# Optimization experiments

Measured on AMD Instinct MI355X. Metric: run time of the kernel, lower is better.

Reference implementation:

```python
import jax, jax.numpy as jnp
import numpy as np

B, L, D, H = 8, 256, 512, 512
NEG_BIG = 1e8  # matches the 100000000.0 mask constant in the original


def setup_inputs() -> dict:
    key = jax.random.key(0)
    k1, k2, k3, k4 = jax.random.split(key, 4)
    enc = jax.random.normal(k1, (B, L, D), dtype=jnp.float32)
    # Glorot-uniform init, matching tf.keras.initializers.GlorotUniform
    s_w = float(np.sqrt(6.0 / (D + H)))
    W_l = jax.random.uniform(k2, (D, H), jnp.float32, -s_w, s_w)
    W_r = jax.random.uniform(k3, (D, H), jnp.float32, -s_w, s_w)
    s_u = float(np.sqrt(6.0 / (H + H)))  # 1-D glorot: fan_in = fan_out = H
    U = jax.random.uniform(k4, (H,), jnp.float32, -s_u, s_u)
    logit_bias = jnp.zeros((1,), jnp.float32)  # bias_initial_value=None -> zeros init
    return {"encoder_output": enc, "W_l": W_l, "W_r": W_r, "U": U, "logit_bias": logit_bias}


def reference(encoder_output, W_l, W_r, U, logit_bias):
    # dot_l[b,i,h], dot_r[b,j,h]
    dot_l = jnp.einsum('bik,kh->bih', encoder_output, W_l)
    dot_r = jnp.einsum('bjk,kh->bjh', encoder_output, W_r)
    # additive biaffine: tanh(dot_l_i + dot_r_j) . U  -> logits[b,i,j]
    final_sum = jnp.tanh(dot_l[:, :, None, :] + dot_r[:, None, :, :])  # [B,L,L,H]
    logits = jnp.einsum('bijh,h->bij', final_sum, U) + logit_bias[0]   # [B,L,L]
    # per-row self-mask (one_hot(i)) applied over all rows at once
    masked = logits - NEG_BIG * jnp.eye(L, dtype=logits.dtype)[None]   # [B,L,L]
    # original returns python lists over i of [B,L]; stack -> [L,B,L]
    mask_scores = jnp.transpose(masked, (1, 0, 2))
    p = jax.nn.sigmoid(mask_scores)
    samples = jax.random.bernoulli(jax.random.key(42), p).astype(jnp.int32)  # [L,B,L]
    # Bernoulli entropy from logits x: p*softplus(-x) + (1-p)*softplus(x)
    entropy = p * jax.nn.softplus(-mask_scores) + (1.0 - p) * jax.nn.softplus(mask_scores)
    return samples, mask_scores, entropy
```

## Files before the change

kernel.cpp:

```cpp
#include <hip/hip_runtime.h>
#include <stdint.h>

#define Bb 8
#define Ll 256
#define Dd 512
#define Hh 512
#define Nout (Ll * Bb * Ll)

#define Kc 2.8853900817779268

#define RNG_PARTITIONABLE 1

typedef __attribute__((ext_vector_type(8))) short bf16x8;
typedef __attribute__((ext_vector_type(4))) float f32x4;


__device__ __forceinline__ uint32_t rotl32(uint32_t v, int s) {
  return (v << s) | (v >> (32 - s));
}
__device__ __forceinline__ void tf_round(uint32_t& x0, uint32_t& x1, int r) {
  x0 += x1;
  x1 = rotl32(x1, r);
  x1 ^= x0;
}
__device__ __forceinline__ uint2 threefry2x32_k042(uint32_t x0, uint32_t x1) {
  const uint32_t k0 = 0u;
  const uint32_t k1 = 42u;
  const uint32_t k2 = 0x1BD11BDAu ^ k0 ^ k1;
  x0 += k0; x1 += k1;
  tf_round(x0, x1, 13); tf_round(x0, x1, 15); tf_round(x0, x1, 26); tf_round(x0, x1, 6);
  x0 += k1; x1 += k2 + 1u;
  tf_round(x0, x1, 17); tf_round(x0, x1, 29); tf_round(x0, x1, 16); tf_round(x0, x1, 24);
  x0 += k2; x1 += k0 + 2u;
  tf_round(x0, x1, 13); tf_round(x0, x1, 15); tf_round(x0, x1, 26); tf_round(x0, x1, 6);
  x0 += k0; x1 += k1 + 3u;
  tf_round(x0, x1, 17); tf_round(x0, x1, 29); tf_round(x0, x1, 16); tf_round(x0, x1, 24);
  x0 += k1; x1 += k2 + 4u;
  tf_round(x0, x1, 13); tf_round(x0, x1, 15); tf_round(x0, x1, 26); tf_round(x0, x1, 6);
  x0 += k2; x1 += k0 + 5u;
  return make_uint2(x0, x1);
}

__device__ __forceinline__ uint32_t rng_bits(uint32_t n) {
#if RNG_PARTITIONABLE
  uint2 o = threefry2x32_k042(0u, n);
  return o.x ^ o.y;
#else
  const uint32_t half = (uint32_t)(Nout / 2);
  if (n < half) {
    uint2 o = threefry2x32_k042(n, n + half);
    return o.x;
  } else {
    uint2 o = threefry2x32_k042(n - half, n);
    return o.y;
  }
#endif
}

__device__ __forceinline__ unsigned short bf16_rne(float f) {
  uint32_t u = __float_as_uint(f);
  u = (u + 0x7fffu + ((u >> 16) & 1u)) >> 16;
  return (unsigned short)u;
}
__device__ __forceinline__ float bf16_tof(unsigned short h) {
  return __uint_as_float(((uint32_t)h) << 16);
}
__device__ __forceinline__ void split3(float a, unsigned short& h,
                                       unsigned short& m, unsigned short& l) {
  h = bf16_rne(a);
  const float r1 = a - bf16_tof(h);
  m = bf16_rne(r1);
  const float r2 = r1 - bf16_tof(m);
  l = bf16_rne(r2);
}

__device__ __forceinline__ uint32_t fp_off(int r, int k) {
  const int mt = r >> 4, l15 = r & 15;
  const int kc = k >> 5, kq = (k >> 3) & 3, j = k & 7;
  return (uint32_t)(mt * 8192 + kc * 512 + kq * 128 + l15 * 8 + j);
}

__global__ __launch_bounds__(256) void split_enc(
    const float* __restrict__ enc, unsigned short* __restrict__ ah,
    unsigned short* __restrict__ am, unsigned short* __restrict__ al) {
  const int idx = (blockIdx.x * 256 + threadIdx.x) * 4;
  const int r = idx >> 9;
  const int k = idx & 511;
  const float4 v = *(const float4*)(enc + idx);
  ushort4 h4, m4, l4;
  split3(v.x, h4.x, m4.x, l4.x);
  split3(v.y, h4.y, m4.y, l4.y);
  split3(v.z, h4.z, m4.z, l4.z);
  split3(v.w, h4.w, m4.w, l4.w);
  const uint32_t o = fp_off(r, k);
  *(ushort4*)(ah + o) = h4;
  *(ushort4*)(am + o) = m4;
  *(ushort4*)(al + o) = l4;
}

__global__ __launch_bounds__(256) void split_wt(
    const float* __restrict__ Wl, const float* __restrict__ Wr,
    unsigned short* __restrict__ wh, unsigned short* __restrict__ wm,
    unsigned short* __restrict__ wl) {
  const int z = blockIdx.z;
  const float* W = z ? Wr : Wl;
  const uint32_t zo = (uint32_t)z * Hh * Dd;
  const int k0 = blockIdx.x * 64;
  const int n0 = blockIdx.y * 64;
  __shared__ float tile[64][65];

  const int t = threadIdx.x;
#pragma unroll
  for (int rep = 0; rep < 4; ++rep) {
    const int idx = t + rep * 256;
    const int r = idx >> 4;
    const int c = (idx & 15) * 4;
    const float4 v = *(const float4*)(W + (size_t)(k0 + r) * Hh + n0 + c);
    tile[r][c + 0] = v.x; tile[r][c + 1] = v.y;
    tile[r][c + 2] = v.z; tile[r][c + 3] = v.w;
  }
  __syncthreads();
#pragma unroll
  for (int rep = 0; rep < 4; ++rep) {
    const int idx = t + rep * 256;
    const int rr = idx >> 4;
    const int cc = (idx & 15) * 4;
    ushort4 h4, m4, l4;
    split3(tile[cc + 0][rr], h4.x, m4.x, l4.x);
    split3(tile[cc + 1][rr], h4.y, m4.y, l4.y);
    split3(tile[cc + 2][rr], h4.z, m4.z, l4.z);
    split3(tile[cc + 3][rr], h4.w, m4.w, l4.w);
    const uint32_t o = zo + fp_off(n0 + rr, k0 + cc);
    *(ushort4*)(wh + o) = h4;
    *(ushort4*)(wm + o) = m4;
    *(ushort4*)(wl + o) = l4;
  }
}

__global__ __launch_bounds__(256) void gemm_mfma(
    const unsigned short* __restrict__ ah, const unsigned short* __restrict__ am,
    const unsigned short* __restrict__ al, const unsigned short* __restrict__ wh,
    const unsigned short* __restrict__ wm, const unsigned short* __restrict__ wl,
    float* __restrict__ el, float* __restrict__ er) {
  const int flat = blockIdx.x;
  const int xcd = flat & 7;
  const int loc = flat >> 3;
  const int z = loc >> 5;
  const int ni = (loc >> 2) & 7;
  const int mi = (xcd << 2) | (loc & 3);
  float* C = z ? er : el;
  const int m0 = mi * 64;
  const int n0 = ni * 64;

  __shared__ unsigned short Asm[2][12 * 512];
  __shared__ unsigned short Bsm[2][12 * 512];

  const int t = threadIdx.x;
  const int lane = t & 63;
  const int wv = t >> 6;
  const int l15 = lane & 15;

  const unsigned short* gp[6];
  uint32_t go[6];
  int lq[6];
  bool isA[6];
#pragma unroll
  for (int s = 0; s < 6; ++s) {
    const int q = wv * 6 + s;
    if (q < 12) {
      const int p = q >> 2, mt = q & 3;
      gp[s] = (p == 0) ? ah : (p == 1) ? am : al;
      go[s] = (uint32_t)(mi * 4 + mt) * 8192u + (uint32_t)lane * 8u;
      lq[s] = q * 512;
      isA[s] = true;
    } else {
      const int q2 = q - 12;
      const int p = q2 >> 2, nt = q2 & 3;
      gp[s] = (p == 0) ? wh : (p == 1) ? wm : wl;
      go[s] = (uint32_t)z * 262144u + (uint32_t)(ni * 4 + nt) * 8192u +
              (uint32_t)lane * 8u;
      lq[s] = q2 * 512;
      isA[s] = false;
    }
  }

  auto stage = [&](int buf, int kc) {
    const uint32_t k0 = (uint32_t)kc * 512u;
#pragma unroll
    for (int s = 0; s < 6; ++s) {
      unsigned short* dst = isA[s] ? &Asm[buf][lq[s]] : &Bsm[buf][lq[s]];
      __builtin_amdgcn_global_load_lds(
          (const __attribute__((address_space(1))) void*)(gp[s] + go[s] + k0),
          (__attribute__((address_space(3))) void*)dst, 16, 0, 0);
    }
  };

  const int mp = wv & 1;
  const int np = wv >> 1;

  f32x4 acc[2][2][2];
#pragma unroll
  for (int mi2 = 0; mi2 < 2; ++mi2)
#pragma unroll
    for (int ni2 = 0; ni2 < 2; ++ni2)
#pragma unroll
      for (int hf = 0; hf < 2; ++hf) acc[mi2][ni2][hf] = (f32x4){0.f, 0.f, 0.f, 0.f};

  stage(0, 0);
  __syncthreads();

  for (int kc = 0; kc < 16; ++kc) {
    const int buf = kc & 1;
    if (kc < 15) stage(buf ^ 1, kc + 1);

    bf16x8 af[2][3], bfr[2][3];
#pragma unroll
    for (int mi2 = 0; mi2 < 2; ++mi2)
#pragma unroll
      for (int p = 0; p < 3; ++p)
        af[mi2][p] = *(const bf16x8*)&Asm[buf][(p * 4 + mp * 2 + mi2) * 512 + lane * 8];
#pragma unroll
    for (int ni2 = 0; ni2 < 2; ++ni2)
#pragma unroll
      for (int p = 0; p < 3; ++p)
        bfr[ni2][p] = *(const bf16x8*)&Bsm[buf][(p * 4 + np * 2 + ni2) * 512 + lane * 8];

    const int hf = kc >> 3;
#pragma unroll
    for (int mi2 = 0; mi2 < 2; ++mi2)
#pragma unroll
      for (int ni2 = 0; ni2 < 2; ++ni2) {
        f32x4 A = acc[mi2][ni2][hf];
        A = __builtin_amdgcn_mfma_f32_16x16x32_bf16(af[mi2][0], bfr[ni2][0], A, 0, 0, 0);
        A = __builtin_amdgcn_mfma_f32_16x16x32_bf16(af[mi2][0], bfr[ni2][1], A, 0, 0, 0);
        A = __builtin_amdgcn_mfma_f32_16x16x32_bf16(af[mi2][1], bfr[ni2][0], A, 0, 0, 0);
        A = __builtin_amdgcn_mfma_f32_16x16x32_bf16(af[mi2][0], bfr[ni2][2], A, 0, 0, 0);
        A = __builtin_amdgcn_mfma_f32_16x16x32_bf16(af[mi2][2], bfr[ni2][0], A, 0, 0, 0);
        A = __builtin_amdgcn_mfma_f32_16x16x32_bf16(af[mi2][1], bfr[ni2][1], A, 0, 0, 0);
        acc[mi2][ni2][hf] = A;
      }
    __syncthreads();
  }

  const int rbase = (lane >> 4) * 4;
#pragma unroll
  for (int mi2 = 0; mi2 < 2; ++mi2) {
    const int mbase = m0 + (mp * 2 + mi2) * 16 + rbase;
#pragma unroll
    for (int ni2 = 0; ni2 < 2; ++ni2) {
      const int n = n0 + (np * 2 + ni2) * 16 + l15;
#pragma unroll
      for (int reg = 0; reg < 4; ++reg) {
        const double s = (double)acc[mi2][ni2][0][reg] + (double)acc[mi2][ni2][1][reg];
        C[(size_t)(mbase + reg) * Hh + n] = __builtin_amdgcn_exp2f((float)(Kc * s));
      }
    }
  }
}

__device__ __forceinline__ void group4_acc(float& S, const float4 a,
                                           const float4 bv, const float4 u) {
  const float d0 = __builtin_fmaf(a.x, bv.x, 1.0f);
  const float d1 = __builtin_fmaf(a.y, bv.y, 1.0f);
  const float d2 = __builtin_fmaf(a.z, bv.z, 1.0f);
  const float d3 = __builtin_fmaf(a.w, bv.w, 1.0f);
  const float p01 = d0 * d1;
  const float p23 = d2 * d3;
  const float D = p01 * p23;
  float n01 = u.x * d1;
  n01 = __builtin_fmaf(u.y, d0, n01);
  float n23 = u.z * d3;
  n23 = __builtin_fmaf(u.w, d2, n23);
  float num = n01 * p23;
  num = __builtin_fmaf(n23, p01, num);
  S = __builtin_fmaf(num, __builtin_amdgcn_rcpf(D), S);
}

__global__ __launch_bounds__(256) void biaffine_part(
    const float* __restrict__ el, const float* __restrict__ er,
    const float* __restrict__ U, float* __restrict__ part) {
  const int flat = blockIdx.x;
  const int b = flat & 7;
  const int loc = flat >> 3;
  const int ks = loc >> 4;
  const int ib = (loc >> 2) & 3;
  const int jb = loc & 3;
  const int i0 = ib * 64;
  const int j0 = jb * 64;
  const int h0 = ks * 64;

  __shared__ float els[64][68];
  __shared__ float ers[64][68];
  __shared__ float us[64];

  const int t = threadIdx.x;
  if (t < 16) *(float4*)&us[t * 4] = *(const float4*)(U + h0 + t * 4);

  const float* elg = el + (size_t)(b * Ll + i0) * Hh + h0;
  const float* erg = er + (size_t)(b * Ll + j0) * Hh + h0;
#pragma unroll
  for (int rep = 0; rep < 4; ++rep) {
    const int idx = t + rep * 256;
    const int r = idx >> 4;
    const int c = (idx & 15) * 4;
    *(float4*)&els[r][c] = *(const float4*)(elg + (size_t)r * Hh + c);
    *(float4*)&ers[r][c] = *(const float4*)(erg + (size_t)r * Hh + c);
  }
  __syncthreads();

  float usl = 0.0f;
#pragma unroll
  for (int q = 0; q < 16; ++q) {
    const float4 u = *(const float4*)&us[q * 4];
    usl += ((u.x + u.y) + u.z) + u.w;
  }

  const int ti = t >> 4;
  const int tj = t & 15;

  float S[4][4];
#pragma unroll
  for (int r = 0; r < 4; ++r)
#pragma unroll
    for (int c = 0; c < 4; ++c) S[r][c] = 0.0f;

  for (int g = 0; g < 16; ++g) {
    const int h = g * 4;
    const float4 u = *(const float4*)&us[h];
    float4 av[4], bv[4];
#pragma unroll
    for (int c = 0; c < 4; ++c) {
      av[c] = *(const float4*)&els[ti + 16 * c][h];
      bv[c] = *(const float4*)&ers[tj + 16 * c][h];
    }
#pragma unroll
    for (int r = 0; r < 4; ++r)
#pragma unroll
      for (int c = 0; c < 4; ++c) group4_acc(S[r][c], av[r], bv[c], u);
  }

  float* pslice = part + (size_t)ks * Nout;
#pragma unroll
  for (int r = 0; r < 4; ++r) {
    const int i = i0 + ti + 16 * r;
#pragma unroll
    for (int c = 0; c < 4; ++c) {
      const int j = j0 + tj + 16 * c;
      const uint32_t n = ((uint32_t)i * Bb + (uint32_t)b) * Ll + (uint32_t)j;
      pslice[n] = __builtin_fmaf(-2.0f, S[r][c], usl);
    }
  }
}

__global__ __launch_bounds__(256) void biaffine_emit(
    const float* __restrict__ part, const float* __restrict__ biasp,
    float* __restrict__ out) {
  const uint32_t n4 = (blockIdx.x * 256u + threadIdx.x) * 4u;
  double s0 = 0.0, s1 = 0.0, s2 = 0.0, s3 = 0.0;
#pragma unroll
  for (int k = 0; k < 8; ++k) {
    const float4 v = *(const float4*)(part + (size_t)k * Nout + n4);
    s0 += (double)v.x;
    s1 += (double)v.y;
    s2 += (double)v.z;
    s3 += (double)v.w;
  }
  const float bias = biasp[0];
  const double sv[4] = {s0, s1, s2, s3};

  float4 samp4, x4, ent4;
  float* sp = &samp4.x;
  float* xp = &x4.x;
  float* ep = &ent4.x;
#pragma unroll
  for (int q = 0; q < 4; ++q) {
    const uint32_t n = n4 + q;
    const int i = (int)(n >> 11);
    const int j = (int)(n & 255u);
    float x = (float)sv[q] + bias;
    if (i == j) x -= 1e8f;

    const double pd = 1.0 / (1.0 + exp(-(double)x));
    const float pf = (float)pd;

    const uint32_t bits = rng_bits(n);
    const float uu = __uint_as_float((bits >> 9) | 0x3f800000u) - 1.0f;
    sp[q] = (uu < pf) ? 1.0f : 0.0f;
    xp[q] = x;

    const float ax = fabsf(x);
    const float l1p = log1pf(expf(-ax));
    const float sp_pos = fmaxf(x, 0.0f) + l1p;
    const float sp_neg = fmaxf(-x, 0.0f) + l1p;
    ep[q] = pf * sp_neg + (1.0f - pf) * sp_pos;
  }
  *(float4*)(out + n4) = samp4;
  *(float4*)(out + Nout + n4) = x4;
  *(float4*)(out + 2 * (size_t)Nout + n4) = ent4;
}

extern "C" void kernel_launch(void* const* d_in, const int* in_sizes, int n_in,
                              void* d_out, int out_size, void* d_ws,
                              size_t ws_size, hipStream_t stream) {
  const float* enc = (const float*)d_in[0];
  const float* Wl = (const float*)d_in[1];
  const float* Wr = (const float*)d_in[2];
  const float* U = (const float*)d_in[3];
  const float* lb = (const float*)d_in[4];
  float* out = (float*)d_out;

  char* w = (char*)d_ws;
  float* el = (float*)w;                      w += (size_t)Bb * Ll * Hh * 4;
  float* er = (float*)w;                      w += (size_t)Bb * Ll * Hh * 4;
  float* part = (float*)w;                    w += (size_t)8 * Nout * 4;
  unsigned short* ah = (unsigned short*)w;    w += (size_t)Bb * Ll * Dd * 2;
  unsigned short* am = (unsigned short*)w;    w += (size_t)Bb * Ll * Dd * 2;
  unsigned short* al = (unsigned short*)w;    w += (size_t)Bb * Ll * Dd * 2;
  unsigned short* wh = (unsigned short*)w;    w += (size_t)2 * Dd * Hh * 2;
  unsigned short* wm = (unsigned short*)w;    w += (size_t)2 * Dd * Hh * 2;
  unsigned short* wl = (unsigned short*)w;    w += (size_t)2 * Dd * Hh * 2;

  split_enc<<<dim3((Bb * Ll * Dd) / 1024), 256, 0, stream>>>(enc, ah, am, al);
  split_wt<<<dim3(Dd / 64, Hh / 64, 2), 256, 0, stream>>>(Wl, Wr, wh, wm, wl);
  gemm_mfma<<<dim3(512, 1, 1), 256, 0, stream>>>(
      ah, am, al, wh, wm, wl, el, er);
  biaffine_part<<<dim3(1024, 1, 1), 256, 0, stream>>>(el, er, U, part);
  biaffine_emit<<<dim3(Nout / 1024), 256, 0, stream>>>(part, lb, out);
}
```

Measured before the change: 115.7 us.

## Merge split kernels, change partial-sum layout to b-major, unroll biaffine loop

Fuses the encoder and weight bf16-splitting kernels into one launch by dispatching on block index, which removes a kernel launch. The biaffine partial buffer is re-indexed in [b,i,j] order so each block's stores are contiguous, and the emit kernel reads that layout and scatters to the [i,b,j] output. It also adds unroll-2 on the inner h-group loop. The fused kernel reserves shared memory even for the encoder blocks, and the emit kernel now writes to less regular output positions.

New measurement: 119.8 us. 3.5% more time.

```diff
diff --git a/kernel.cpp b/kernel.cpp
--- a/kernel.cpp
+++ b/kernel.cpp
@@ -80,36 +80,43 @@
   return (uint32_t)(mt * 8192 + kc * 512 + kq * 128 + l15 * 8 + j);
 }
 
-__global__ __launch_bounds__(256) void split_enc(
-    const float* __restrict__ enc, unsigned short* __restrict__ ah,
-    unsigned short* __restrict__ am, unsigned short* __restrict__ al) {
-  const int idx = (blockIdx.x * 256 + threadIdx.x) * 4;
-  const int r = idx >> 9;
-  const int k = idx & 511;
-  const float4 v = *(const float4*)(enc + idx);
-  ushort4 h4, m4, l4;
-  split3(v.x, h4.x, m4.x, l4.x);
-  split3(v.y, h4.y, m4.y, l4.y);
-  split3(v.z, h4.z, m4.z, l4.z);
-  split3(v.w, h4.w, m4.w, l4.w);
-  const uint32_t o = fp_off(r, k);
-  *(ushort4*)(ah + o) = h4;
-  *(ushort4*)(am + o) = m4;
-  *(ushort4*)(al + o) = l4;
-}
-
-__global__ __launch_bounds__(256) void split_wt(
-    const float* __restrict__ Wl, const float* __restrict__ Wr,
+__global__ __launch_bounds__(256) void split_all(
+    const float* __restrict__ enc, const float* __restrict__ Wl,
+    const float* __restrict__ Wr, unsigned short* __restrict__ ah,
+    unsigned short* __restrict__ am, unsigned short* __restrict__ al,
     unsigned short* __restrict__ wh, unsigned short* __restrict__ wm,
     unsigned short* __restrict__ wl) {
-  const int z = blockIdx.z;
+  __shared__ float tile[64][65];
+  const int bx = blockIdx.x;
+  const int t = threadIdx.x;
+
+  if (bx < 1024) {
+    const int idx = (bx * 256 + t) * 4;
+    const int r = idx >> 9;
+    const int k = idx & 511;
+    const float4 v = *(const float4*)(enc + idx);
+    ushort4 h4, m4, l4;
+    split3(v.x, h4.x, m4.x, l4.x);
+    split3(v.y, h4.y, m4.y, l4.y);
+    split3(v.z, h4.z, m4.z, l4.z);
+    split3(v.w, h4.w, m4.w, l4.w);
+    const uint32_t o = fp_off(r, k);
+    *(ushort4*)(ah + o) = h4;
+    *(ushort4*)(am + o) = m4;
+    *(ushort4*)(al + o) = l4;
+    return;
+  }
+
+  const int id = bx - 1024;
+  const int z = id >> 6;
+  const int rest = id & 63;
+  const int kb = rest >> 3;
+  const int nb = rest & 7;
   const float* W = z ? Wr : Wl;
   const uint32_t zo = (uint32_t)z * Hh * Dd;
-  const int k0 = blockIdx.x * 64;
-  const int n0 = blockIdx.y * 64;
-  __shared__ float tile[64][65];
-
-  const int t = threadIdx.x;
+  const int k0 = kb * 64;
+  const int n0 = nb * 64;
+
 #pragma unroll
   for (int rep = 0; rep < 4; ++rep) {
     const int idx = t + rep * 256;
@@ -324,6 +331,7 @@
 #pragma unroll
     for (int c = 0; c < 4; ++c) S[r][c] = 0.0f;
 
+#pragma unroll 2
   for (int g = 0; g < 16; ++g) {
     const int h = g * 4;
     const float4 u = *(const float4*)&us[h];
@@ -346,8 +354,8 @@
 #pragma unroll
     for (int c = 0; c < 4; ++c) {
       const int j = j0 + tj + 16 * c;
-      const uint32_t n = ((uint32_t)i * Bb + (uint32_t)b) * Ll + (uint32_t)j;
-      pslice[n] = __builtin_fmaf(-2.0f, S[r][c], usl);
+      const uint32_t m = ((uint32_t)b << 16) | ((uint32_t)i << 8) | (uint32_t)j;
+      pslice[m] = __builtin_fmaf(-2.0f, S[r][c], usl);
     }
   }
 }
@@ -355,11 +363,16 @@
 __global__ __launch_bounds__(256) void biaffine_emit(
     const float* __restrict__ part, const float* __restrict__ biasp,
     float* __restrict__ out) {
-  const uint32_t n4 = (blockIdx.x * 256u + threadIdx.x) * 4u;
+  const int flat = blockIdx.x;
+  const int b = flat & 7;
+  const int loc = flat >> 3;
+  const uint32_t mi4 = (uint32_t)loc * 1024u + (uint32_t)threadIdx.x * 4u;
+  const uint32_t mbase = ((uint32_t)b << 16) | mi4;
+
   double s0 = 0.0, s1 = 0.0, s2 = 0.0, s3 = 0.0;
 #pragma unroll
   for (int k = 0; k < 8; ++k) {
-    const float4 v = *(const float4*)(part + (size_t)k * Nout + n4);
+    const float4 v = *(const float4*)(part + (size_t)k * Nout + mbase);
     s0 += (double)v.x;
     s1 += (double)v.y;
     s2 += (double)v.z;
@@ -368,15 +381,18 @@
   const float bias = biasp[0];
   const double sv[4] = {s0, s1, s2, s3};
 
+  const int i = (int)(mi4 >> 8);
+  const int jb = (int)(mi4 & 255u);
+  const uint32_t nb = (((uint32_t)i * Bb + (uint32_t)b) << 8) | (uint32_t)jb;
+
   float4 samp4, x4, ent4;
   float* sp = &samp4.x;
   float* xp = &x4.x;
   float* ep = &ent4.x;
 #pragma unroll
   for (int q = 0; q < 4; ++q) {
-    const uint32_t n = n4 + q;
-    const int i = (int)(n >> 11);
-    const int j = (int)(n & 255u);
+    const uint32_t n = nb + q;
+    const int j = jb + q;
     float x = (float)sv[q] + bias;
     if (i == j) x -= 1e8f;
 
@@ -394,9 +410,9 @@
     const float sp_neg = fmaxf(-x, 0.0f) + l1p;
     ep[q] = pf * sp_neg + (1.0f - pf) * sp_pos;
   }
-  *(float4*)(out + n4) = samp4;
-  *(float4*)(out + Nout + n4) = x4;
-  *(float4*)(out + 2 * (size_t)Nout + n4) = ent4;
+  *(float4*)(out + nb) = samp4;
+  *(float4*)(out + Nout + nb) = x4;
+  *(float4*)(out + 2 * (size_t)Nout + nb) = ent4;
 }
 
 extern "C" void kernel_launch(void* const* d_in, const int* in_sizes, int n_in,
@@ -420,10 +436,10 @@
   unsigned short* wm = (unsigned short*)w;    w += (size_t)2 * Dd * Hh * 2;
   unsigned short* wl = (unsigned short*)w;    w += (size_t)2 * Dd * Hh * 2;
 
-  split_enc<<<dim3((Bb * Ll * Dd) / 1024), 256, 0, stream>>>(enc, ah, am, al);
-  split_wt<<<dim3(Dd / 64, Hh / 64, 2), 256, 0, stream>>>(Wl, Wr, wh, wm, wl);
+  split_all<<<dim3(1024 + 128), 256, 0, stream>>>(enc, Wl, Wr, ah, am, al,
+                                                  wh, wm, wl);
   gemm_mfma<<<dim3(512, 1, 1), 256, 0, stream>>>(
       ah, am, al, wh, wm, wl, el, er);
   biaffine_part<<<dim3(1024, 1, 1), 256, 0, stream>>>(el, er, U, part);
-  biaffine_emit<<<dim3(Nout / 1024), 256, 0, stream>>>(part, lb, out);
-}
+  biaffine_emit<<<dim3(512, 1, 1), 256, 0, stream>>>(part, lb, out);
+}
```
